# Kernel optimization log

Measured on AMD Instinct MI355X. Metric: run time of the kernel, lower is better.

## Reference

```python
import jax, jax.numpy as jnp
import numpy as np

N, K, D = 262144, 1024, 64

def setup_inputs() -> dict:
    key = jax.random.key(0)
    k1, k2 = jax.random.split(key)
    previous_residual = jax.random.normal(k1, (N, D), dtype=jnp.float32)
    # GlorotUniform over (K, D): limit = sqrt(6/(K+D))
    limit = np.sqrt(6.0 / (K + D)).astype(np.float32)
    codebook_embeddings = jax.random.uniform(k2, (K, D), dtype=jnp.float32, minval=-limit, maxval=limit)
    return {"previous_residual": previous_residual, "codebook_embeddings": codebook_embeddings}

def reference(previous_residual, codebook_embeddings):
    x_sq = jnp.sum(previous_residual * previous_residual, axis=-1, keepdims=True)  # [N,1]
    c_sq = jnp.sum(codebook_embeddings * codebook_embeddings, axis=-1)             # [K]
    xc = jnp.einsum('nd,kd->nk', previous_residual, codebook_embeddings)           # [N,K]
    distances = x_sq - 2.0 * xc + c_sq[None, :]
    closest_codebook_index = jnp.argmin(distances, axis=1)                          # [N] int
    codebook_embedding = codebook_embeddings[closest_codebook_index]                # [N,D]
    next_residual = previous_residual - codebook_embedding
    return (closest_codebook_index, next_residual, codebook_embedding)
```

## Files before the change

### kernel.cpp

```cpp
#include <hip/hip_runtime.h>
#include <math.h>

#define N_ROWS 262144
#define K_CODES 1024
#define D_DIM 64
#define WL_CAP 65536

typedef __attribute__((ext_vector_type(8))) short short8;
typedef __attribute__((ext_vector_type(4))) float f32x4;
typedef unsigned short ushortT;
typedef unsigned int uintT;

__device__ inline uintT bf16_rne_bits(float v) {
    uintT u = __float_as_uint(v);
    return (u + 0x7FFFu + ((u >> 16) & 1u)) >> 16;
}

__global__ __launch_bounds__(256) void prep_kernel(const float* __restrict__ cb,
                                                   ushortT* __restrict__ cbh,
                                                   ushortT* __restrict__ cbl,
                                                   float* __restrict__ c_sq,
                                                   int* __restrict__ cnt) {
    if (blockIdx.x == 0 && threadIdx.x == 0) *cnt = 0;
    int k = blockIdx.x * 256 + threadIdx.x;
    if (k >= K_CODES) return;
    const float4* row = (const float4*)(cb + (size_t)k * D_DIM);
    float s = 0.0f;
#pragma unroll
    for (int j = 0; j < D_DIM / 4; ++j) {
        float4 v = row[j];
        s = fmaf(v.x, v.x, s);
        s = fmaf(v.y, v.y, s);
        s = fmaf(v.z, v.z, s);
        s = fmaf(v.w, v.w, s);
        float e[4] = {v.x, v.y, v.z, v.w};
#pragma unroll
        for (int q = 0; q < 4; ++q) {
            int d = 4 * j + q;
            uintT hb = bf16_rne_bits(e[q]);
            float hif = __uint_as_float(hb << 16);
            uintT lb = bf16_rne_bits(e[q] - hif);
            cbh[(size_t)k * D_DIM + d] = (ushortT)hb;
            cbl[(size_t)k * D_DIM + d] = (ushortT)lb;
        }
    }
    c_sq[k] = s;
}

__global__ __launch_bounds__(256, 3) void coarse_kernel(
        const float* __restrict__ x_all, const float* __restrict__ cb,
        const ushortT* __restrict__ cbh, const ushortT* __restrict__ cbl,
        const float* __restrict__ c_sq_g,
        float* __restrict__ out_idx, float* __restrict__ out_res,
        float* __restrict__ out_emb, int* __restrict__ cnt,
        int* __restrict__ wl) {
    __shared__ uint4 stage4[2048];
    __shared__ float csq_s[128];
    __shared__ float xsq_s[128];
    __shared__ int   idx_s[128];
    ushortT* stage = (ushortT*)stage4;

    const int t  = threadIdx.x;
    const int w  = t >> 6;
    const int L  = t & 63;
    const int q  = L >> 4;
    const int n  = L & 15;
    const int rowbase = blockIdx.x * 128 + w * 32;

    short8 ah[2][2], al[2][2];
#pragma unroll
    for (int s = 0; s < 2; ++s) {
        float part = 0.0f;
#pragma unroll
        for (int kt = 0; kt < 2; ++kt) {
            const float4* p = (const float4*)(x_all +
                (size_t)(rowbase + s * 16 + n) * D_DIM + kt * 32 + q * 8);
            float4 v0 = p[0], v1 = p[1];
            float e[8] = {v0.x, v0.y, v0.z, v0.w, v1.x, v1.y, v1.z, v1.w};
#pragma unroll
            for (int j = 0; j < 8; ++j) {
                part = fmaf(e[j], e[j], part);
                uintT hb = bf16_rne_bits(e[j]);
                float hif = __uint_as_float(hb << 16);
                uintT lb = bf16_rne_bits(e[j] - hif);
                ah[s][kt][j] = (short)hb;
                al[s][kt][j] = (short)lb;
            }
        }
        part += __shfl_xor(part, 16);
        part += __shfl_xor(part, 32);
        if (q == 0) xsq_s[w * 32 + s * 16 + n] = part;
    }

    float m1[2][4], m2[2][4];
    int   ix[2][4];
#pragma unroll
    for (int s = 0; s < 2; ++s)
#pragma unroll
        for (int j = 0; j < 4; ++j) { m1[s][j] = 3.4e38f; m2[s][j] = 3.4e38f; ix[s][j] = 0; }

    uint4 pre[8];
    float cpre = 0.0f;
#pragma unroll
    for (int it = 0; it < 8; ++it) {
        int chunk = it * 256 + t;
        int tile = chunk >> 8, c = chunk & 255;
        int hilo = (c >> 7) & 1, cc = c & 127;
        int kt = cc >> 6, LL = cc & 63;
        const ushortT* src = hilo ? cbl : cbh;
        size_t elem = (size_t)(tile * 16 + (LL & 15)) * D_DIM + kt * 32 + (LL >> 4) * 8;
        pre[it] = *(const uint4*)(src + elem);
    }
    if (t < 128) cpre = c_sq_g[t];

    for (int r = 0; r < 8; ++r) {
        __syncthreads();
#pragma unroll
        for (int it = 0; it < 8; ++it)
            *(uint4*)(stage + (it * 256 + t) * 8) = pre[it];
        if (t < 128) csq_s[t] = cpre;
        __syncthreads();

        if (r < 7) {
            int rn = r + 1;
#pragma unroll
            for (int it = 0; it < 8; ++it) {
                int chunk = it * 256 + t;
                int tile = chunk >> 8, c = chunk & 255;
                int hilo = (c >> 7) & 1, cc = c & 127;
                int kt = cc >> 6, LL = cc & 63;
                const ushortT* src = hilo ? cbl : cbh;
                size_t elem = (size_t)(rn * 128 + tile * 16 + (LL & 15)) * D_DIM +
                              kt * 32 + (LL >> 4) * 8;
                pre[it] = *(const uint4*)(src + elem);
            }
            if (t < 128) cpre = c_sq_g[rn * 128 + t];
        }

#pragma unroll
        for (int tl = 0; tl < 8; ++tl) {
            const int tb = tl * 2048;
            short8 bh0 = *(const short8*)(stage + tb +        0 * 512 + L * 8);
            short8 bh1 = *(const short8*)(stage + tb +        1 * 512 + L * 8);
            short8 bl0 = *(const short8*)(stage + tb + 1024 + 0 * 512 + L * 8);
            short8 bl1 = *(const short8*)(stage + tb + 1024 + 1 * 512 + L * 8);

            f32x4 acc0 = {0.f, 0.f, 0.f, 0.f};
            f32x4 acc1 = {0.f, 0.f, 0.f, 0.f};
            acc0 = __builtin_amdgcn_mfma_f32_16x16x32_bf16(ah[0][0], bh0, acc0, 0, 0, 0);
            acc1 = __builtin_amdgcn_mfma_f32_16x16x32_bf16(ah[1][0], bh0, acc1, 0, 0, 0);
            acc0 = __builtin_amdgcn_mfma_f32_16x16x32_bf16(ah[0][1], bh1, acc0, 0, 0, 0);
            acc1 = __builtin_amdgcn_mfma_f32_16x16x32_bf16(ah[1][1], bh1, acc1, 0, 0, 0);
            acc0 = __builtin_amdgcn_mfma_f32_16x16x32_bf16(ah[0][0], bl0, acc0, 0, 0, 0);
            acc1 = __builtin_amdgcn_mfma_f32_16x16x32_bf16(ah[1][0], bl0, acc1, 0, 0, 0);
            acc0 = __builtin_amdgcn_mfma_f32_16x16x32_bf16(ah[0][1], bl1, acc0, 0, 0, 0);
            acc1 = __builtin_amdgcn_mfma_f32_16x16x32_bf16(ah[1][1], bl1, acc1, 0, 0, 0);
            acc0 = __builtin_amdgcn_mfma_f32_16x16x32_bf16(al[0][0], bh0, acc0, 0, 0, 0);
            acc1 = __builtin_amdgcn_mfma_f32_16x16x32_bf16(al[1][0], bh0, acc1, 0, 0, 0);
            acc0 = __builtin_amdgcn_mfma_f32_16x16x32_bf16(al[0][1], bh1, acc0, 0, 0, 0);
            acc1 = __builtin_amdgcn_mfma_f32_16x16x32_bf16(al[1][1], bh1, acc1, 0, 0, 0);

            float cv = csq_s[tl * 16 + n];
            int kc = r * 128 + tl * 16 + n;
#pragma unroll
            for (int j = 0; j < 4; ++j) {
                float d0 = fmaf(-2.0f, acc0[j], cv);
                bool lt0 = d0 < m1[0][j];
                m2[0][j] = lt0 ? m1[0][j] : fminf(m2[0][j], d0);
                m1[0][j] = lt0 ? d0 : m1[0][j];
                ix[0][j] = lt0 ? kc : ix[0][j];
                float d1 = fmaf(-2.0f, acc1[j], cv);
                bool lt1 = d1 < m1[1][j];
                m2[1][j] = lt1 ? m1[1][j] : fminf(m2[1][j], d1);
                m1[1][j] = lt1 ? d1 : m1[1][j];
                ix[1][j] = lt1 ? kc : ix[1][j];
            }
        }
    }

#pragma unroll
    for (int s = 0; s < 2; ++s)
#pragma unroll
        for (int j = 0; j < 4; ++j) {
            float a1 = m1[s][j], a2 = m2[s][j];
            int ai = ix[s][j];
#pragma unroll
            for (int msk = 1; msk < 16; msk <<= 1) {
                float o1 = __shfl_xor(a1, msk);
                float o2 = __shfl_xor(a2, msk);
                int oi = __shfl_xor(ai, msk);
                float nm2 = fminf(fmaxf(a1, o1), fminf(a2, o2));
                bool take = (o1 < a1) || (o1 == a1 && oi < ai);
                a1 = take ? o1 : a1;
                ai = take ? oi : ai;
                a2 = nm2;
            }
            m1[s][j] = a1; m2[s][j] = a2; ix[s][j] = ai;
        }

    if (n == 0) {
#pragma unroll
        for (int s = 0; s < 2; ++s)
#pragma unroll
            for (int j = 0; j < 4; ++j) {
                int rl = w * 32 + s * 16 + q * 4 + j;
                float xn = sqrtf(xsq_s[rl]);
                float margin = fmaf(4.0e-5f, xn, 2.0e-4f);
                bool fb = (m2[s][j] - m1[s][j]) <= 2.0f * margin;
                idx_s[rl] = ix[s][j] | (fb ? (1 << 30) : 0);
            }
    }
    __syncthreads();

    if (t < 128) {
        int e = idx_s[t];
        int row = blockIdx.x * 128 + t;
        out_idx[row] = (float)(e & 0x3FFFFFFF);
        if (e >> 30) {
            int pos = atomicAdd(cnt, 1);
            if (pos < WL_CAP) wl[pos] = row;
        }
    }
    {
        int row = blockIdx.x * 128 + (t >> 1);
        int seg = (t & 1) * 32;
        int id = idx_s[t >> 1] & 0x3FFFFFFF;
        const float4* xs = (const float4*)(x_all + (size_t)row * D_DIM + seg);
        const float4* cs = (const float4*)(cb + (size_t)id * D_DIM + seg);
        float4* rs = (float4*)(out_res + (size_t)row * D_DIM + seg);
        float4* es = (float4*)(out_emb + (size_t)row * D_DIM + seg);
#pragma unroll
        for (int j = 0; j < 8; ++j) {
            float4 xv = xs[j], cv = cs[j];
            float4 rv;
            rv.x = xv.x - cv.x; rv.y = xv.y - cv.y;
            rv.z = xv.z - cv.z; rv.w = xv.w - cv.w;
            rs[j] = rv;
            es[j] = cv;
        }
    }
}

__global__ __launch_bounds__(256) void fallback_kernel(
        const float* __restrict__ x_all, const float* __restrict__ cb,
        const float* __restrict__ c_sq, const int* __restrict__ wl,
        const int* __restrict__ cnt,
        float* __restrict__ out_idx, float* __restrict__ out_res,
        float* __restrict__ out_emb) {
    int count = *cnt;
    if (count > WL_CAP) count = WL_CAP;
    const int L = threadIdx.x & 63;
    const int waveId = blockIdx.x * 4 + (threadIdx.x >> 6);
    const int nWaves = gridDim.x * 4;

    for (int i = waveId; i < count; i += nWaves) {
        int r = wl[i];

        float x[D_DIM];
        const float4* xr = (const float4*)(x_all + (size_t)r * D_DIM);
#pragma unroll
        for (int j = 0; j < D_DIM / 4; ++j) {
            float4 v = xr[j];
            x[4 * j + 0] = v.x; x[4 * j + 1] = v.y;
            x[4 * j + 2] = v.z; x[4 * j + 3] = v.w;
        }
        float x_sq = 0.0f;
#pragma unroll
        for (int d = 0; d < D_DIM; ++d) x_sq = fmaf(x[d], x[d], x_sq);

        float best = INFINITY;
        int bidx = 0x7FFFFFFF;
        for (int kk = 0; kk < 16; ++kk) {
            int k = kk * 64 + L;
            const float* c0 = cb + (size_t)k * D_DIM;
            float a00 = 0.f, a01 = 0.f, a02 = 0.f, a03 = 0.f;
#pragma unroll
            for (int j = 0; j < 4; ++j) {
                float4 v0 = *(const float4*)(c0 + 16 * j + 0);
                float4 v1 = *(const float4*)(c0 + 16 * j + 4);
                float4 v2 = *(const float4*)(c0 + 16 * j + 8);
                float4 v3 = *(const float4*)(c0 + 16 * j + 12);
                float* a = (j == 0) ? &a00 : (j == 1) ? &a01 : (j == 2) ? &a02 : &a03;
                float acc = *a;
                acc = fmaf(x[16 * j + 0],  v0.x, acc);
                acc = fmaf(x[16 * j + 1],  v0.y, acc);
                acc = fmaf(x[16 * j + 2],  v0.z, acc);
                acc = fmaf(x[16 * j + 3],  v0.w, acc);
                acc = fmaf(x[16 * j + 4],  v1.x, acc);
                acc = fmaf(x[16 * j + 5],  v1.y, acc);
                acc = fmaf(x[16 * j + 6],  v1.z, acc);
                acc = fmaf(x[16 * j + 7],  v1.w, acc);
                acc = fmaf(x[16 * j + 8],  v2.x, acc);
                acc = fmaf(x[16 * j + 9],  v2.y, acc);
                acc = fmaf(x[16 * j + 10], v2.z, acc);
                acc = fmaf(x[16 * j + 11], v2.w, acc);
                acc = fmaf(x[16 * j + 12], v3.x, acc);
                acc = fmaf(x[16 * j + 13], v3.y, acc);
                acc = fmaf(x[16 * j + 14], v3.z, acc);
                acc = fmaf(x[16 * j + 15], v3.w, acc);
                *a = acc;
            }
            float dot = (a00 + a01) + (a02 + a03);
            float d = (x_sq - 2.0f * dot) + c_sq[k];
            if (d < best) { best = d; bidx = k; }
        }

#pragma unroll
        for (int msk = 1; msk < 64; msk <<= 1) {
            float ob = __shfl_xor(best, msk);
            int oi = __shfl_xor(bidx, msk);
            bool take = (ob < best) || (ob == best && oi < bidx);
            best = take ? ob : best;
            bidx = take ? oi : bidx;
        }

        if (L < 16) {
            const float4* cbest = (const float4*)(cb + (size_t)bidx * D_DIM);
            float4 c = cbest[L];
            float4 v;
            v.x = x[4 * L + 0] - c.x; v.y = x[4 * L + 1] - c.y;
            v.z = x[4 * L + 2] - c.z; v.w = x[4 * L + 3] - c.w;
            ((float4*)(out_res + (size_t)r * D_DIM))[L] = v;
            ((float4*)(out_emb + (size_t)r * D_DIM))[L] = c;
            if (L == 0) out_idx[r] = (float)bidx;
        }
    }
}

extern "C" void kernel_launch(void* const* d_in, const int* in_sizes, int n_in,
                              void* d_out, int out_size, void* d_ws, size_t ws_size,
                              hipStream_t stream) {
    const float* x  = (const float*)d_in[0];
    const float* cb = (const float*)d_in[1];

    char* base = (char*)d_ws;
    ushortT* cbh = (ushortT*)base;
    ushortT* cbl = (ushortT*)(base + 131072);
    float*   csq = (float*)(base + 262144);
    int*     cnt = (int*)(base + 266240);
    int*     wl  = (int*)(base + 266256);

    float* out   = (float*)d_out;
    float* o_idx = out;
    float* o_res = out + (size_t)N_ROWS;
    float* o_emb = o_res + (size_t)N_ROWS * D_DIM;

    prep_kernel<<<4, 256, 0, stream>>>(cb, cbh, cbl, csq, cnt);
    coarse_kernel<<<N_ROWS / 128, 256, 0, stream>>>(x, cb, cbh, cbl, csq,
                                                    o_idx, o_res, o_emb, cnt, wl);
    fallback_kernel<<<1024, 256, 0, stream>>>(x, cb, csq, wl, cnt,
                                              o_idx, o_res, o_emb);
}
```

Baseline: 497.3 us.

## Stream codebook fragments from L2 into registers and pack argmin index into distance bits

The per-block LDS staging of the bf16 hi/lo codebook, with its barriers, is replaced by direct per-lane register loads from global memory, double-buffered across pairs of 16-code tiles. The running top-2 search now packs the tile index into the low 6 mantissa bits of a negated distance, so each update is a pair of integer max/min operations. The fallback threshold is widened to absorb that lost precision, and rows with large norms always take the fallback. The input rows are also cached in LDS so the epilogue does not re-read them, occupancy is raised to 4 blocks, and the worklist capacity grows. All of this trades LDS traffic and synchronisation for more L2 reads and a possibly larger fallback workload.

```diff
diff --git a/kernel.cpp b/kernel.cpp
--- a/kernel.cpp
+++ b/kernel.cpp
@@ -4,7 +4,7 @@
 #define N_ROWS 262144
 #define K_CODES 1024
 #define D_DIM 64
-#define WL_CAP 65536
+#define WL_CAP 262144
 
 typedef __attribute__((ext_vector_type(8))) short short8;
 typedef __attribute__((ext_vector_type(4))) float f32x4;
@@ -16,13 +16,13 @@
     return (u + 0x7FFFu + ((u >> 16) & 1u)) >> 16;
 }
 
-__global__ __launch_bounds__(256) void prep_kernel(const float* __restrict__ cb,
-                                                   ushortT* __restrict__ cbh,
-                                                   ushortT* __restrict__ cbl,
-                                                   float* __restrict__ c_sq,
-                                                   int* __restrict__ cnt) {
+__global__ __launch_bounds__(64) void prep_kernel(const float* __restrict__ cb,
+                                                  ushortT* __restrict__ cbh,
+                                                  ushortT* __restrict__ cbl,
+                                                  float* __restrict__ c_sq,
+                                                  int* __restrict__ cnt) {
     if (blockIdx.x == 0 && threadIdx.x == 0) *cnt = 0;
-    int k = blockIdx.x * 256 + threadIdx.x;
+    int k = blockIdx.x * 64 + threadIdx.x;
     if (k >= K_CODES) return;
     const float4* row = (const float4*)(cb + (size_t)k * D_DIM);
     float s = 0.0f;
@@ -47,18 +47,17 @@
     c_sq[k] = s;
 }
 
-__global__ __launch_bounds__(256, 3) void coarse_kernel(
+__global__ __launch_bounds__(256, 4) void coarse_kernel(
         const float* __restrict__ x_all, const float* __restrict__ cb,
         const ushortT* __restrict__ cbh, const ushortT* __restrict__ cbl,
         const float* __restrict__ c_sq_g,
         float* __restrict__ out_idx, float* __restrict__ out_res,
         float* __restrict__ out_emb, int* __restrict__ cnt,
         int* __restrict__ wl) {
-    __shared__ uint4 stage4[2048];
-    __shared__ float csq_s[128];
+    __shared__ float xs_s[128][68];
+    __shared__ float csq_s[K_CODES];
     __shared__ float xsq_s[128];
     __shared__ int   idx_s[128];
-    ushortT* stage = (ushortT*)stage4;
 
     const int t  = threadIdx.x;
     const int w  = t >> 6;
@@ -67,6 +66,19 @@
     const int n  = L & 15;
     const int rowbase = blockIdx.x * 128 + w * 32;
 
+    const ushortT* bh_base = cbh + (size_t)n * D_DIM + q * 8;
+    const ushortT* bl_base = cbl + (size_t)n * D_DIM + q * 8;
+    short8 a_h0 = *(const short8*)(bh_base + 0);
+    short8 a_h1 = *(const short8*)(bh_base + 32);
+    short8 a_l0 = *(const short8*)(bl_base + 0);
+    short8 a_l1 = *(const short8*)(bl_base + 32);
+    short8 b_h0 = *(const short8*)(bh_base + 1024);
+    short8 b_h1 = *(const short8*)(bh_base + 1024 + 32);
+    short8 b_l0 = *(const short8*)(bl_base + 1024);
+    short8 b_l1 = *(const short8*)(bl_base + 1024 + 32);
+
+    ((float4*)csq_s)[t] = ((const float4*)c_sq_g)[t];
+
     short8 ah[2][2], al[2][2];
 #pragma unroll
     for (int s = 0; s < 2; ++s) {
@@ -76,6 +88,9 @@
             const float4* p = (const float4*)(x_all +
                 (size_t)(rowbase + s * 16 + n) * D_DIM + kt * 32 + q * 8);
             float4 v0 = p[0], v1 = p[1];
+            int lr = w * 32 + s * 16 + n;
+            *(float4*)&xs_s[lr][kt * 32 + q * 8] = v0;
+            *(float4*)&xs_s[lr][kt * 32 + q * 8 + 4] = v1;
             float e[8] = {v0.x, v0.y, v0.z, v0.w, v1.x, v1.y, v1.z, v1.w};
 #pragma unroll
             for (int j = 0; j < 8; ++j) {
@@ -91,90 +106,62 @@
         part += __shfl_xor(part, 32);
         if (q == 0) xsq_s[w * 32 + s * 16 + n] = part;
     }
-
-    float m1[2][4], m2[2][4];
-    int   ix[2][4];
+    __syncthreads();
+
+    int m1p[2][4], m2p[2][4];
 #pragma unroll
     for (int s = 0; s < 2; ++s)
 #pragma unroll
-        for (int j = 0; j < 4; ++j) { m1[s][j] = 3.4e38f; m2[s][j] = 3.4e38f; ix[s][j] = 0; }
-
-    uint4 pre[8];
-    float cpre = 0.0f;
-#pragma unroll
-    for (int it = 0; it < 8; ++it) {
-        int chunk = it * 256 + t;
-        int tile = chunk >> 8, c = chunk & 255;
-        int hilo = (c >> 7) & 1, cc = c & 127;
-        int kt = cc >> 6, LL = cc & 63;
-        const ushortT* src = hilo ? cbl : cbh;
-        size_t elem = (size_t)(tile * 16 + (LL & 15)) * D_DIM + kt * 32 + (LL >> 4) * 8;
-        pre[it] = *(const uint4*)(src + elem);
-    }
-    if (t < 128) cpre = c_sq_g[t];
-
-    for (int r = 0; r < 8; ++r) {
-        __syncthreads();
-#pragma unroll
-        for (int it = 0; it < 8; ++it)
-            *(uint4*)(stage + (it * 256 + t) * 8) = pre[it];
-        if (t < 128) csq_s[t] = cpre;
-        __syncthreads();
-
-        if (r < 7) {
-            int rn = r + 1;
-#pragma unroll
-            for (int it = 0; it < 8; ++it) {
-                int chunk = it * 256 + t;
-                int tile = chunk >> 8, c = chunk & 255;
-                int hilo = (c >> 7) & 1, cc = c & 127;
-                int kt = cc >> 6, LL = cc & 63;
-                const ushortT* src = hilo ? cbl : cbh;
-                size_t elem = (size_t)(rn * 128 + tile * 16 + (LL & 15)) * D_DIM +
-                              kt * 32 + (LL >> 4) * 8;
-                pre[it] = *(const uint4*)(src + elem);
-            }
-            if (t < 128) cpre = c_sq_g[rn * 128 + t];
-        }
-
-#pragma unroll
-        for (int tl = 0; tl < 8; ++tl) {
-            const int tb = tl * 2048;
-            short8 bh0 = *(const short8*)(stage + tb +        0 * 512 + L * 8);
-            short8 bh1 = *(const short8*)(stage + tb +        1 * 512 + L * 8);
-            short8 bl0 = *(const short8*)(stage + tb + 1024 + 0 * 512 + L * 8);
-            short8 bl1 = *(const short8*)(stage + tb + 1024 + 1 * 512 + L * 8);
-
-            f32x4 acc0 = {0.f, 0.f, 0.f, 0.f};
-            f32x4 acc1 = {0.f, 0.f, 0.f, 0.f};
-            acc0 = __builtin_amdgcn_mfma_f32_16x16x32_bf16(ah[0][0], bh0, acc0, 0, 0, 0);
-            acc1 = __builtin_amdgcn_mfma_f32_16x16x32_bf16(ah[1][0], bh0, acc1, 0, 0, 0);
-            acc0 = __builtin_amdgcn_mfma_f32_16x16x32_bf16(ah[0][1], bh1, acc0, 0, 0, 0);
-            acc1 = __builtin_amdgcn_mfma_f32_16x16x32_bf16(ah[1][1], bh1, acc1, 0, 0, 0);
-            acc0 = __builtin_amdgcn_mfma_f32_16x16x32_bf16(ah[0][0], bl0, acc0, 0, 0, 0);
-            acc1 = __builtin_amdgcn_mfma_f32_16x16x32_bf16(ah[1][0], bl0, acc1, 0, 0, 0);
-            acc0 = __builtin_amdgcn_mfma_f32_16x16x32_bf16(ah[0][1], bl1, acc0, 0, 0, 0);
-            acc1 = __builtin_amdgcn_mfma_f32_16x16x32_bf16(ah[1][1], bl1, acc1, 0, 0, 0);
-            acc0 = __builtin_amdgcn_mfma_f32_16x16x32_bf16(al[0][0], bh0, acc0, 0, 0, 0);
-            acc1 = __builtin_amdgcn_mfma_f32_16x16x32_bf16(al[1][0], bh0, acc1, 0, 0, 0);
-            acc0 = __builtin_amdgcn_mfma_f32_16x16x32_bf16(al[0][1], bh1, acc0, 0, 0, 0);
-            acc1 = __builtin_amdgcn_mfma_f32_16x16x32_bf16(al[1][1], bh1, acc1, 0, 0, 0);
-
-            float cv = csq_s[tl * 16 + n];
-            int kc = r * 128 + tl * 16 + n;
-#pragma unroll
-            for (int j = 0; j < 4; ++j) {
-                float d0 = fmaf(-2.0f, acc0[j], cv);
-                bool lt0 = d0 < m1[0][j];
-                m2[0][j] = lt0 ? m1[0][j] : fminf(m2[0][j], d0);
-                m1[0][j] = lt0 ? d0 : m1[0][j];
-                ix[0][j] = lt0 ? kc : ix[0][j];
-                float d1 = fmaf(-2.0f, acc1[j], cv);
-                bool lt1 = d1 < m1[1][j];
-                m2[1][j] = lt1 ? m1[1][j] : fminf(m2[1][j], d1);
-                m1[1][j] = lt1 ? d1 : m1[1][j];
-                ix[1][j] = lt1 ? kc : ix[1][j];
-            }
+        for (int j = 0; j < 4; ++j) { m1p[s][j] = (int)0x80000000; m2p[s][j] = (int)0x80000000; }
+
+    auto tile_step = [&](int tl, const short8& bh0, const short8& bh1,
+                         const short8& bl0, const short8& bl1) {
+        f32x4 acc0 = {0.f, 0.f, 0.f, 0.f};
+        f32x4 acc1 = {0.f, 0.f, 0.f, 0.f};
+        acc0 = __builtin_amdgcn_mfma_f32_16x16x32_bf16(ah[0][0], bh0, acc0, 0, 0, 0);
+        acc1 = __builtin_amdgcn_mfma_f32_16x16x32_bf16(ah[1][0], bh0, acc1, 0, 0, 0);
+        acc0 = __builtin_amdgcn_mfma_f32_16x16x32_bf16(ah[0][1], bh1, acc0, 0, 0, 0);
+        acc1 = __builtin_amdgcn_mfma_f32_16x16x32_bf16(ah[1][1], bh1, acc1, 0, 0, 0);
+        acc0 = __builtin_amdgcn_mfma_f32_16x16x32_bf16(ah[0][0], bl0, acc0, 0, 0, 0);
+        acc1 = __builtin_amdgcn_mfma_f32_16x16x32_bf16(ah[1][0], bl0, acc1, 0, 0, 0);
+        acc0 = __builtin_amdgcn_mfma_f32_16x16x32_bf16(ah[0][1], bl1, acc0, 0, 0, 0);
+        acc1 = __builtin_amdgcn_mfma_f32_16x16x32_bf16(ah[1][1], bl1, acc1, 0, 0, 0);
+        acc0 = __builtin_amdgcn_mfma_f32_16x16x32_bf16(al[0][0], bh0, acc0, 0, 0, 0);
+        acc1 = __builtin_amdgcn_mfma_f32_16x16x32_bf16(al[1][0], bh0, acc1, 0, 0, 0);
+        acc0 = __builtin_amdgcn_mfma_f32_16x16x32_bf16(al[0][1], bh1, acc0, 0, 0, 0);
+        acc1 = __builtin_amdgcn_mfma_f32_16x16x32_bf16(al[1][1], bh1, acc1, 0, 0, 0);
+
+        float cv = csq_s[tl * 16 + n];
+        uintT kcp = (uintT)(63 - tl);
+#pragma unroll
+        for (int j = 0; j < 4; ++j) {
+            float v0 = fmaf(2.0f, acc0[j], -cv);
+            int u0 = (int)((__float_as_uint(v0) & 0xFFFFFFC0u) | kcp);
+            m2p[0][j] = max(m2p[0][j], min(m1p[0][j], u0));
+            m1p[0][j] = max(m1p[0][j], u0);
+            float v1 = fmaf(2.0f, acc1[j], -cv);
+            int u1 = (int)((__float_as_uint(v1) & 0xFFFFFFC0u) | kcp);
+            m2p[1][j] = max(m2p[1][j], min(m1p[1][j], u1));
+            m1p[1][j] = max(m1p[1][j], u1);
+        }
+    };
+
+    for (int tl = 0; tl < 64; tl += 2) {
+        tile_step(tl, a_h0, a_h1, a_l0, a_l1);
+        if (tl + 2 < 64) {
+            size_t o = (size_t)(tl + 2) * 1024;
+            a_h0 = *(const short8*)(bh_base + o);
+            a_h1 = *(const short8*)(bh_base + o + 32);
+            a_l0 = *(const short8*)(bl_base + o);
+            a_l1 = *(const short8*)(bl_base + o + 32);
+        }
+        tile_step(tl + 1, b_h0, b_h1, b_l0, b_l1);
+        if (tl + 3 < 64) {
+            size_t o = (size_t)(tl + 3) * 1024;
+            b_h0 = *(const short8*)(bh_base + o);
+            b_h1 = *(const short8*)(bh_base + o + 32);
+            b_l0 = *(const short8*)(bl_base + o);
+            b_l1 = *(const short8*)(bl_base + o + 32);
         }
     }
 
@@ -182,34 +169,30 @@
     for (int s = 0; s < 2; ++s)
 #pragma unroll
         for (int j = 0; j < 4; ++j) {
-            float a1 = m1[s][j], a2 = m2[s][j];
-            int ai = ix[s][j];
+            int p1 = m1p[s][j], p2 = m2p[s][j];
+            float a1 = __uint_as_float((uintT)p1 & 0xFFFFFFC0u);
+            float a2 = __uint_as_float((uintT)p2 & 0xFFFFFFC0u);
+            int ai = ((63 - (p1 & 63)) << 4) | n;
 #pragma unroll
             for (int msk = 1; msk < 16; msk <<= 1) {
                 float o1 = __shfl_xor(a1, msk);
                 float o2 = __shfl_xor(a2, msk);
                 int oi = __shfl_xor(ai, msk);
-                float nm2 = fminf(fmaxf(a1, o1), fminf(a2, o2));
-                bool take = (o1 < a1) || (o1 == a1 && oi < ai);
+                float nm2 = fmaxf(fminf(a1, o1), fmaxf(a2, o2));
+                bool take = (o1 > a1) || (o1 == a1 && oi < ai);
                 a1 = take ? o1 : a1;
                 ai = take ? oi : ai;
                 a2 = nm2;
             }
-            m1[s][j] = a1; m2[s][j] = a2; ix[s][j] = ai;
-        }
-
-    if (n == 0) {
-#pragma unroll
-        for (int s = 0; s < 2; ++s)
-#pragma unroll
-            for (int j = 0; j < 4; ++j) {
+            if (n == 0) {
                 int rl = w * 32 + s * 16 + q * 4 + j;
-                float xn = sqrtf(xsq_s[rl]);
-                float margin = fmaf(4.0e-5f, xn, 2.0e-4f);
-                bool fb = (m2[s][j] - m1[s][j]) <= 2.0f * margin;
-                idx_s[rl] = ix[s][j] | (fb ? (1 << 30) : 0);
+                float xsq = xsq_s[rl];
+                float xn = sqrtf(xsq);
+                float thr = fmaf(8.0e-5f, xn, 6.44140625e-4f);
+                bool fb = ((a1 - a2) <= thr) || (a2 < 0.0f) || (xsq > 170.0f);
+                idx_s[rl] = ai | (fb ? (1 << 30) : 0);
             }
-    }
+        }
     __syncthreads();
 
     if (t < 128) {
@@ -222,16 +205,18 @@
         }
     }
     {
-        int row = blockIdx.x * 128 + (t >> 1);
+        int lr = t >> 1;
+        int row = blockIdx.x * 128 + lr;
         int seg = (t & 1) * 32;
-        int id = idx_s[t >> 1] & 0x3FFFFFFF;
-        const float4* xs = (const float4*)(x_all + (size_t)row * D_DIM + seg);
+        int id = idx_s[lr] & 0x3FFFFFFF;
+        const float* xrow = &xs_s[lr][seg];
         const float4* cs = (const float4*)(cb + (size_t)id * D_DIM + seg);
         float4* rs = (float4*)(out_res + (size_t)row * D_DIM + seg);
         float4* es = (float4*)(out_emb + (size_t)row * D_DIM + seg);
 #pragma unroll
         for (int j = 0; j < 8; ++j) {
-            float4 xv = xs[j], cv = cs[j];
+            float4 xv = *(const float4*)(xrow + 4 * j);
+            float4 cv = cs[j];
             float4 rv;
             rv.x = xv.x - cv.x; rv.y = xv.y - cv.y;
             rv.z = xv.z - cv.z; rv.w = xv.w - cv.w;
@@ -345,7 +330,7 @@
     float* o_res = out + (size_t)N_ROWS;
     float* o_emb = o_res + (size_t)N_ROWS * D_DIM;
 
-    prep_kernel<<<4, 256, 0, stream>>>(cb, cbh, cbl, csq, cnt);
+    prep_kernel<<<16, 64, 0, stream>>>(cb, cbh, cbl, csq, cnt);
     coarse_kernel<<<N_ROWS / 128, 256, 0, stream>>>(x, cb, cbh, cbl, csq,
                                                     o_idx, o_res, o_emb, cnt, wl);
     fallback_kernel<<<1024, 256, 0, stream>>>(x, cb, csq, wl, cnt,
```

Result: faster. 482.3 us (-3.0%).
